# Optimization experiments

Hardware: AMD Instinct MI355X
Metric: run time of the kernel (lower is better)

Reference implementation:

```python
import jax, jax.numpy as jnp
import numpy as np

N, C, H, W = 8, 128, 56, 56
CO = C // 8  # 16


def setup_inputs() -> dict:
    key = jax.random.key(0)
    k1, k2, k3, k4 = jax.random.split(key, 4)
    x = jax.random.normal(k1, (N, C, H, W), dtype=jnp.float32)
    # p_3: Conv2d(c*35 -> c//8, 1x1). The unfold channel order is (c, kh=5, kw=7),
    # so the 1x1 conv over c*35 channels is exactly a dilated 5x7 conv with
    # weight [CO, C, 5, 7] and rhs_dilation (2, 3).
    w3 = jax.random.normal(k2, (CO, C, 5, 7), dtype=jnp.float32) * 0.02
    w4 = jax.random.normal(k3, (CO, CO), dtype=jnp.float32) * 0.1
    w5 = jax.random.normal(k4, (C, CO), dtype=jnp.float32) * 0.1
    return {"x": x, "w3": w3, "w4": w4, "w5": w5}


def reference(x, w3, w4, w5):
    # Fused equivalent of: unfold(5x1, dil 2, pad 4) -> unfold(1x7, dil 3, pad 9)
    # -> 1x1 conv (c*35 -> c//8). Padding (4,4)/(9,9) keeps 'same' spatial size.
    y = jax.lax.conv_general_dilated(
        x, w3,
        window_strides=(1, 1),
        padding=((4, 4), (9, 9)),
        rhs_dilation=(2, 3),
        dimension_numbers=("NCHW", "OIHW", "NCHW"),
    )  # [N, CO, H, W]
    y = jnp.einsum("oc,nchw->nohw", w4, y)  # p_4: 1x1 conv CO->CO
    y = jnp.einsum("oc,nchw->nohw", w5, y)  # p_5: 1x1 conv CO->C
    return y
```

## Files before the change

kernel.cpp:

```cpp
#include <hip/hip_runtime.h>

#define BN 8
#define BC 128
#define BH 56
#define BW 56
#define HW 3136
#define NTAP 35
#define WS_WC 71680
#define WS_XP (WS_WC + 4096)
#define XROW 2368

typedef unsigned short u16;
typedef unsigned int u32;
typedef __bf16 bf16x8 __attribute__((ext_vector_type(8)));
typedef float f32x4 __attribute__((ext_vector_type(4)));

__device__ __forceinline__ u16 f2b(float f) {
    unsigned u = __float_as_uint(f);
    return (u16)((u + 0x7FFFu + ((u >> 16) & 1u)) >> 16);
}
__device__ __forceinline__ u32 pack2(float a, float b) {
    return (u32)f2b(a) | ((u32)f2b(b) << 16);
}
__device__ __forceinline__ void dma16(const void* g, void* l) {
    __builtin_amdgcn_global_load_lds(
        (const __attribute__((address_space(1))) u32*)g,
        (__attribute__((address_space(3))) u32*)l, 16, 0, 0);
}

__global__ __launch_bounds__(256) void prep_all(
    const float* __restrict__ x, const float* __restrict__ w3,
    const float* __restrict__ w4, const float* __restrict__ w5,
    u16* __restrict__ ws)
{
    const int b = blockIdx.x;
    const int tid = threadIdx.x;

    if (b >= 2048) {
        int i = (b - 2048) * 256 + tid;
        if (i < WS_WC) {
            int j = i & 7, lane = (i >> 3) & 63, r = i >> 9;
            int tap = r % NTAP, cc = r / NTAP;
            int q = lane >> 4, lm = lane & 15;
            ws[i] = f2b(w3[(lm * BC + cc * 32 + q * 8 + j) * NTAP + tap]);
        } else if (i < WS_WC + 4096) {
            int i2 = i - WS_WC;
            int j = i2 & 7, lane = (i2 >> 3) & 63, ot = i2 >> 9;
            int q = lane >> 4, lm = lane & 15, o = ot * 16 + lm, k = q * 8 + j;
            float s = 0.f;
            if (k < 16)
                for (int c = 0; c < 16; ++c) s += w5[o * 16 + c] * w4[c * 16 + k];
            ws[i] = f2b(s);
        }
        return;
    }

    __shared__ float ls[32][57];
    const int hp = b & 63, cc = (b >> 6) & 3, n = b >> 8;
    u32* dst = (u32*)(ws + WS_XP + (size_t)((n * 4 + cc) * 64 + hp) * XROW);
    const int gr = hp - 4;

    if ((unsigned)gr >= BH) {
        for (int i = tid; i < XROW / 2; i += 256) dst[i] = 0u;
        return;
    }
    for (int i = tid; i < 32 * 14; i += 256) {
        int c = i / 14, w4i = i % 14;
        float4 v = *(const float4*)(x + ((size_t)(n * BC + cc * 32 + c) * BH + gr) * BW + 4 * w4i);
        ls[c][4 * w4i + 0] = v.x;
        ls[c][4 * w4i + 1] = v.y;
        ls[c][4 * w4i + 2] = v.z;
        ls[c][4 * w4i + 3] = v.w;
    }
    __syncthreads();
    for (int i = tid; i < 74 * 16; i += 256) {
        int col = i >> 4, cp = i & 15;
        int gw = col - 9;
        u32 v = 0u;
        if ((unsigned)gw < BW) v = pack2(ls[2 * cp][gw], ls[2 * cp + 1][gw]);
        dst[col * 16 + cp] = v;
    }
}

#define XSBUF 25600
#define XS_OFF 0
#define Y3_OFF 51200
#define SMEM_SZ 56320

__global__ __launch_bounds__(512, 4) void conv_mfma(
    const u16* __restrict__ wsT, float* __restrict__ out)
{
    __shared__ __align__(16) char smem[SMEM_SZ];
    u16* y3T = (u16*)(smem + Y3_OFF);
    float* cbuf = (float*)(smem + XS_OFF);

    const int n = blockIdx.x & 7;
    const int h = blockIdx.x >> 3;
    const int tid = threadIdx.x, lane = tid & 63, wv = tid >> 6;
    const int g = wv & 3, wp = wv >> 2;
    const int q = lane >> 4, lm = lane & 15;
    const int c0 = wp * 32 + lm;
    const int c1 = c0 + 16;
    const int t0 = 9 * g;
    const int ntap = (g == 3) ? 8 : 9;

#define STAGE(CC, BUF) do {                                                   \
        const u16* xbase = wsT + WS_XP + (size_t)((n * 4 + (CC)) * 64 + h) * XROW; \
        char* xd = smem + XS_OFF + (BUF) * XSBUF;                             \
        for (int k = wv; k < 25; k += 8) {                                    \
            int r = k / 5, s = k - 5 * r;                                     \
            dma16(xbase + (size_t)(2 * r) * XROW + s * 512 + lane * 8,        \
                  xd + r * 5120 + s * 1024 + lane * 16);                      \
        }                                                                     \
    } while (0)

    f32x4 acc0 = {0.f, 0.f, 0.f, 0.f};
    f32x4 acc1 = {0.f, 0.f, 0.f, 0.f};

    STAGE(0, 0);
    ((u32*)(y3T + (tid >> 3) * 40))[8 + (tid & 7)] = 0u;
    __syncthreads();

    #pragma unroll
    for (int cc = 0; cc < 4; ++cc) {
        const int buf = cc & 1;
        bf16x8 a[9];
        #pragma unroll
        for (int tt = 0; tt < 9; ++tt) {
            if (tt < ntap)
                a[tt] = *(const bf16x8*)(wsT + (size_t)(cc * NTAP + t0 + tt) * 512 + lane * 8);
        }
        if (cc < 3) STAGE(cc + 1, buf ^ 1);
        const u16* xsb = (const u16*)(smem + XS_OFF + buf * XSBUF);
        #pragma unroll
        for (int tt = 0; tt < 9; ++tt) {
            if (tt < ntap) {
                const int t = t0 + tt;
                const int kh = t / 7, kw = t - 7 * kh;
                const u16* xrow = xsb + (size_t)(kh * 80 + 3 * kw) * 32 + q * 8;
                bf16x8 b0 = *(const bf16x8*)(xrow + (size_t)c0 * 32);
                acc0 = __builtin_amdgcn_mfma_f32_16x16x32_bf16(a[tt], b0, acc0, 0, 0, 0);
                bf16x8 b1 = *(const bf16x8*)(xrow + (size_t)c1 * 32);
                acc1 = __builtin_amdgcn_mfma_f32_16x16x32_bf16(a[tt], b1, acc1, 0, 0, 0);
            }
        }
        if (cc < 3) __syncthreads();
    }

    if (g > 0) {
        float* cb = cbuf + (size_t)(((wp * 3 + (g - 1)) * 2) * 64 + lane) * 4;
        *(f32x4*)cb = acc0;
        *(f32x4*)(cb + 256) = acc1;
    }
    __syncthreads();
    if (g == 0) {
        #pragma unroll
        for (int p = 0; p < 3; ++p) {
            const float* cb = cbuf + (size_t)(((wp * 3 + p) * 2) * 64 + lane) * 4;
            f32x4 v0 = *(const f32x4*)cb;
            f32x4 v1 = *(const f32x4*)(cb + 256);
            acc0[0] += v0[0]; acc0[1] += v0[1]; acc0[2] += v0[2]; acc0[3] += v0[3];
            acc1[0] += v1[0]; acc1[1] += v1[1]; acc1[2] += v1[2]; acc1[3] += v1[3];
        }
        const bool ok1 = (c1 < BW);
        *(u32*)(y3T + c0 * 40 + q * 4)     = pack2(acc0[0], acc0[1]);
        *(u32*)(y3T + c0 * 40 + q * 4 + 2) = pack2(acc0[2], acc0[3]);
        *(u32*)(y3T + c1 * 40 + q * 4)     = ok1 ? pack2(acc1[0], acc1[1]) : 0u;
        *(u32*)(y3T + c1 * 40 + q * 4 + 2) = ok1 ? pack2(acc1[2], acc1[3]) : 0u;
    }
    __syncthreads();

    const int ct = wv & 3, og = wv >> 2;
    const int wgc = ct * 16 + lm;
    bf16x8 bfrag = *(const bf16x8*)(y3T + (size_t)wgc * 40 + q * 8);
    #pragma unroll
    for (int i = 0; i < 4; ++i) {
        const int ot = 4 * og + i;
        bf16x8 afrag = *(const bf16x8*)(wsT + WS_WC + (size_t)(ot * 64 + lane) * 8);
        f32x4 c2 = {0.f, 0.f, 0.f, 0.f};
        c2 = __builtin_amdgcn_mfma_f32_16x16x32_bf16(afrag, bfrag, c2, 0, 0, 0);
        if (wgc < BW) {
            const int o = ot * 16 + q * 4;
            float* po = out + ((size_t)(n * BC + o) * BH + h) * BW + wgc;
            po[0]      = c2[0];
            po[HW]     = c2[1];
            po[2 * HW] = c2[2];
            po[3 * HW] = c2[3];
        }
    }
#undef STAGE
}

extern "C" void kernel_launch(void* const* d_in, const int* in_sizes, int n_in,
                              void* d_out, int out_size, void* d_ws, size_t ws_size,
                              hipStream_t stream)
{
    (void)in_sizes; (void)n_in; (void)out_size; (void)ws_size;
    const float* x  = (const float*)d_in[0];
    const float* w3 = (const float*)d_in[1];
    const float* w4 = (const float*)d_in[2];
    const float* w5 = (const float*)d_in[3];
    u16* ws = (u16*)d_ws;

    prep_all<<<2048 + 296, 256, 0, stream>>>(x, w3, w4, w5, ws);
    conv_mfma<<<BN * BH, 512, 0, stream>>>(ws, (float*)d_out);
}
```

Baseline: 88.01 us.

## Fuse input bf16 conversion into conv kernel, loading fp32 x directly

The separate prep pass that converted x to a padded bf16 channel-interleaved layout in workspace is removed. The conv kernel now loads fp32 rows of x into registers, converts and packs them, and writes them to a padded LDS layout with a wider column stride (40 instead of 32 halves), zeroing pad columns and out-of-range rows itself. This drops a global write and re-read of the transformed input plus part of a kernel launch, and double-buffers the register loads against MFMA work. The cost is more LDS, extra conversion work per block that is redundant across blocks sharing rows, and lower occupancy.

```diff
diff --git a/kernel.cpp b/kernel.cpp
--- a/kernel.cpp
+++ b/kernel.cpp
@@ -7,8 +7,6 @@
 #define HW 3136
 #define NTAP 35
 #define WS_WC 71680
-#define WS_XP (WS_WC + 4096)
-#define XROW 2368
 
 typedef unsigned short u16;
 typedef unsigned int u32;
@@ -22,77 +20,41 @@
 __device__ __forceinline__ u32 pack2(float a, float b) {
     return (u32)f2b(a) | ((u32)f2b(b) << 16);
 }
-__device__ __forceinline__ void dma16(const void* g, void* l) {
-    __builtin_amdgcn_global_load_lds(
-        (const __attribute__((address_space(1))) u32*)g,
-        (__attribute__((address_space(3))) u32*)l, 16, 0, 0);
-}
-
-__global__ __launch_bounds__(256) void prep_all(
-    const float* __restrict__ x, const float* __restrict__ w3,
-    const float* __restrict__ w4, const float* __restrict__ w5,
-    u16* __restrict__ ws)
+
+__global__ __launch_bounds__(256) void prep_w(
+    const float* __restrict__ w3, const float* __restrict__ w4,
+    const float* __restrict__ w5, u16* __restrict__ ws)
 {
-    const int b = blockIdx.x;
-    const int tid = threadIdx.x;
-
-    if (b >= 2048) {
-        int i = (b - 2048) * 256 + tid;
-        if (i < WS_WC) {
-            int j = i & 7, lane = (i >> 3) & 63, r = i >> 9;
-            int tap = r % NTAP, cc = r / NTAP;
-            int q = lane >> 4, lm = lane & 15;
-            ws[i] = f2b(w3[(lm * BC + cc * 32 + q * 8 + j) * NTAP + tap]);
-        } else if (i < WS_WC + 4096) {
-            int i2 = i - WS_WC;
-            int j = i2 & 7, lane = (i2 >> 3) & 63, ot = i2 >> 9;
-            int q = lane >> 4, lm = lane & 15, o = ot * 16 + lm, k = q * 8 + j;
-            float s = 0.f;
-            if (k < 16)
-                for (int c = 0; c < 16; ++c) s += w5[o * 16 + c] * w4[c * 16 + k];
-            ws[i] = f2b(s);
-        }
-        return;
-    }
-
-    __shared__ float ls[32][57];
-    const int hp = b & 63, cc = (b >> 6) & 3, n = b >> 8;
-    u32* dst = (u32*)(ws + WS_XP + (size_t)((n * 4 + cc) * 64 + hp) * XROW);
-    const int gr = hp - 4;
-
-    if ((unsigned)gr >= BH) {
-        for (int i = tid; i < XROW / 2; i += 256) dst[i] = 0u;
-        return;
-    }
-    for (int i = tid; i < 32 * 14; i += 256) {
-        int c = i / 14, w4i = i % 14;
-        float4 v = *(const float4*)(x + ((size_t)(n * BC + cc * 32 + c) * BH + gr) * BW + 4 * w4i);
-        ls[c][4 * w4i + 0] = v.x;
-        ls[c][4 * w4i + 1] = v.y;
-        ls[c][4 * w4i + 2] = v.z;
-        ls[c][4 * w4i + 3] = v.w;
-    }
-    __syncthreads();
-    for (int i = tid; i < 74 * 16; i += 256) {
-        int col = i >> 4, cp = i & 15;
-        int gw = col - 9;
-        u32 v = 0u;
-        if ((unsigned)gw < BW) v = pack2(ls[2 * cp][gw], ls[2 * cp + 1][gw]);
-        dst[col * 16 + cp] = v;
-    }
-}
-
-#define XSBUF 25600
-#define XS_OFF 0
-#define Y3_OFF 51200
-#define SMEM_SZ 56320
+    int i = blockIdx.x * 256 + threadIdx.x;
+    if (i < WS_WC) {
+        int j = i & 7, lane = (i >> 3) & 63, r = i >> 9;
+        int tap = r % NTAP, cc = r / NTAP;
+        int q = lane >> 4, lm = lane & 15;
+        ws[i] = f2b(w3[(lm * BC + cc * 32 + q * 8 + j) * NTAP + tap]);
+    } else if (i < WS_WC + 4096) {
+        int i2 = i - WS_WC;
+        int j = i2 & 7, lane = (i2 >> 3) & 63, ot = i2 >> 9;
+        int q = lane >> 4, lm = lane & 15, o = ot * 16 + lm, k = q * 8 + j;
+        float s = 0.f;
+        if (k < 16)
+            for (int c = 0; c < 16; ++c) s += w5[o * 16 + c] * w4[c * 16 + k];
+        ws[i] = f2b(s);
+    }
+}
+
+#define COLW 40
+#define XSBUF 32000
+#define U32BUF 8000
+#define Y3_OFF 64000
+#define SMEM_SZ 69632
 
 __global__ __launch_bounds__(512, 4) void conv_mfma(
-    const u16* __restrict__ wsT, float* __restrict__ out)
+    const float* __restrict__ x, const u16* __restrict__ wsT,
+    float* __restrict__ out)
 {
     __shared__ __align__(16) char smem[SMEM_SZ];
     u16* y3T = (u16*)(smem + Y3_OFF);
-    float* cbuf = (float*)(smem + XS_OFF);
+    float* cbuf = (float*)smem;
 
     const int n = blockIdx.x & 7;
     const int h = blockIdx.x >> 3;
@@ -104,22 +66,70 @@
     const int t0 = 9 * g;
     const int ntap = (g == 3) ? 8 : 9;
 
-#define STAGE(CC, BUF) do {                                                   \
-        const u16* xbase = wsT + WS_XP + (size_t)((n * 4 + (CC)) * 64 + h) * XROW; \
-        char* xd = smem + XS_OFF + (BUF) * XSBUF;                             \
-        for (int k = wv; k < 25; k += 8) {                                    \
-            int r = k / 5, s = k - 5 * r;                                     \
-            dma16(xbase + (size_t)(2 * r) * XROW + s * 512 + lane * 8,        \
-                  xd + r * 5120 + s * 1024 + lane * 16);                      \
+    float4 sa[3], sb[3];
+#define SLOAD(CC) do {                                                        \
+        _Pragma("unroll")                                                     \
+        for (int u = 0; u < 3; ++u) {                                         \
+            int it = tid + u * 512;                                           \
+            if (it < 1120) {                                                  \
+                int r = it / 224, rem = it % 224;                             \
+                int cp = rem / 14, wq = rem % 14;                             \
+                int gr = h - 4 + 2 * r;                                       \
+                if ((unsigned)gr < BH) {                                      \
+                    const float* px = x + ((size_t)(n * BC + (CC) * 32 + 2 * cp) * BH + gr) * BW + 4 * wq; \
+                    sa[u] = *(const float4*)px;                               \
+                    sb[u] = *(const float4*)(px + HW);                        \
+                }                                                             \
+            }                                                                 \
         }                                                                     \
     } while (0)
 
+#define SWRITE(BUF) do {                                                      \
+        u32* xb = (u32*)(smem + (BUF) * XSBUF);                               \
+        _Pragma("unroll")                                                     \
+        for (int u = 0; u < 3; ++u) {                                         \
+            int it = tid + u * 512;                                           \
+            if (it < 1120) {                                                  \
+                int r = it / 224, rem = it % 224;                             \
+                int cp = rem / 14, wq = rem % 14;                             \
+                int gr = h - 4 + 2 * r;                                       \
+                if ((unsigned)gr < BH) {                                      \
+                    u32* d = xb + (r * 80 + 9 + 4 * wq) * 20 + cp;            \
+                    d[0]  = pack2(sa[u].x, sb[u].x);                          \
+                    d[20] = pack2(sa[u].y, sb[u].y);                          \
+                    d[40] = pack2(sa[u].z, sb[u].z);                          \
+                    d[60] = pack2(sa[u].w, sb[u].w);                          \
+                }                                                             \
+            }                                                                 \
+        }                                                                     \
+    } while (0)
+
+    SLOAD(0);
+    for (int i = tid; i < 3840; i += 512) {
+        int cp = i & 15, t = i >> 4;
+        int pc = t % 24, t2 = t / 24;
+        int r = t2 % 5, bb = t2 / 5;
+        int col = pc < 9 ? pc : 56 + pc;
+        ((u32*)smem)[bb * U32BUF + (r * 80 + col) * 20 + cp] = 0u;
+    }
+    int bad0 = 0, bad1 = 0, nb = 0;
+    #pragma unroll
+    for (int r = 0; r < 5; ++r) {
+        int gr = h - 4 + 2 * r;
+        if ((unsigned)gr >= BH) { if (nb == 0) bad0 = r; else bad1 = r; ++nb; }
+    }
+    for (int i = tid; i < nb * 1792; i += 512) {
+        int cp = i & 15, t = i >> 4;
+        int w = t % 56, t2 = t / 56;
+        int bb = t2 & 1, r = (t2 >> 1) ? bad1 : bad0;
+        ((u32*)smem)[bb * U32BUF + (r * 80 + 9 + w) * 20 + cp] = 0u;
+    }
+    ((u32*)(y3T + (tid >> 3) * 40))[8 + (tid & 7)] = 0u;
+    SWRITE(0);
+    __syncthreads();
+
     f32x4 acc0 = {0.f, 0.f, 0.f, 0.f};
     f32x4 acc1 = {0.f, 0.f, 0.f, 0.f};
-
-    STAGE(0, 0);
-    ((u32*)(y3T + (tid >> 3) * 40))[8 + (tid & 7)] = 0u;
-    __syncthreads();
 
     #pragma unroll
     for (int cc = 0; cc < 4; ++cc) {
@@ -130,21 +140,24 @@
             if (tt < ntap)
                 a[tt] = *(const bf16x8*)(wsT + (size_t)(cc * NTAP + t0 + tt) * 512 + lane * 8);
         }
-        if (cc < 3) STAGE(cc + 1, buf ^ 1);
-        const u16* xsb = (const u16*)(smem + XS_OFF + buf * XSBUF);
+        if (cc < 3) SLOAD(cc + 1);
+        const u16* xsb = (const u16*)(smem + buf * XSBUF);
         #pragma unroll
         for (int tt = 0; tt < 9; ++tt) {
             if (tt < ntap) {
                 const int t = t0 + tt;
                 const int kh = t / 7, kw = t - 7 * kh;
-                const u16* xrow = xsb + (size_t)(kh * 80 + 3 * kw) * 32 + q * 8;
-                bf16x8 b0 = *(const bf16x8*)(xrow + (size_t)c0 * 32);
+                const u16* xrow = xsb + (size_t)(kh * 80 + 3 * kw) * COLW + q * 8;
+                bf16x8 b0 = *(const bf16x8*)(xrow + (size_t)c0 * COLW);
                 acc0 = __builtin_amdgcn_mfma_f32_16x16x32_bf16(a[tt], b0, acc0, 0, 0, 0);
-                bf16x8 b1 = *(const bf16x8*)(xrow + (size_t)c1 * 32);
+                bf16x8 b1 = *(const bf16x8*)(xrow + (size_t)c1 * COLW);
                 acc1 = __builtin_amdgcn_mfma_f32_16x16x32_bf16(a[tt], b1, acc1, 0, 0, 0);
             }
         }
-        if (cc < 3) __syncthreads();
+        if (cc < 3) {
+            SWRITE(buf ^ 1);
+            __syncthreads();
+        }
     }
 
     if (g > 0) {
@@ -188,7 +201,8 @@
             po[3 * HW] = c2[3];
         }
     }
-#undef STAGE
+#undef SLOAD
+#undef SWRITE
 }
 
 extern "C" void kernel_launch(void* const* d_in, const int* in_sizes, int n_in,
@@ -202,6 +216,6 @@
     const float* w5 = (const float*)d_in[3];
     u16* ws = (u16*)d_ws;
 
-    prep_all<<<2048 + 296, 256, 0, stream>>>(x, w3, w4, w5, ws);
-    conv_mfma<<<BN * BH, 512, 0, stream>>>(ws, (float*)d_out);
-}
+    prep_w<<<296, 256, 0, stream>>>(w3, w4, w5, ws);
+    conv_mfma<<<BN * BH, 512, 0, stream>>>(x, ws, (float*)d_out);
+}
```

After: 85.17 us, median of 2. -3.2%, faster.
